# Kernel optimization log

Measured on AMD Instinct MI355X. Metric: run time of the kernel, lower is better.

Reference implementation:

```python
import jax, jax.numpy as jnp
import numpy as np

N = 8192
F_IN = 512
H = 512
E = 128
ALPHA = 0.2
NEG = -9e15


def _xavier(key, shape, gain=1.414):
    fan_in, fan_out = shape[0], shape[1]
    bound = gain * np.sqrt(6.0 / (fan_in + fan_out))
    return jax.random.uniform(key, shape, jnp.float32, -bound, bound)


def setup_inputs() -> dict:
    key = jax.random.key(0)
    ks = jax.random.split(key, 9)
    x = jax.random.normal(ks[0], (N, F_IN), jnp.float32)
    u = jax.random.uniform(ks[1], (N, N), jnp.float32)
    adj = jnp.where(u < 0.05, u, 0.0)
    M = jax.random.uniform(ks[2], (N, N), jnp.float32)
    return {
        "x": x, "adj": adj, "M": M,
        "W1": _xavier(ks[3], (F_IN, H)),
        "a_self1": _xavier(ks[4], (H, 1)),
        "a_neigh1": _xavier(ks[5], (H, 1)),
        "W2": _xavier(ks[6], (H, E)),
        "a_self2": _xavier(ks[7], (E, 1)),
        "a_neigh2": _xavier(ks[8], (E, 1)),
    }


def _gat_layer(x, adj, M, W, a_self, a_neigh):
    h = x @ W                                   # (N, out)
    s = h @ a_self                              # (N, 1)
    n = h @ a_neigh                             # (N, 1)
    e = (s + n.T) * M                           # (N, N) broadcast score sum
    e = jnp.where(e > 0, e, ALPHA * e)          # leaky_relu
    masked = jnp.where(adj > 0, e, NEG)
    attn = jax.nn.softmax(masked, axis=1)
    h_prime = attn @ h
    return jax.nn.elu(h_prime)


def reference(x, adj, M, W1, a_self1, a_neigh1, W2, a_self2, a_neigh2):
    h = _gat_layer(x, adj, M, W1, a_self1, a_neigh1)
    h = _gat_layer(h, adj, M, W2, a_self2, a_neigh2)
    z = h / jnp.maximum(jnp.linalg.norm(h, axis=1, keepdims=True), 1e-12)
    A_pred = jax.nn.sigmoid(z @ z.T)
    return (A_pred, z)
```

## Files before the change

kernel.cpp:

```cpp
#include <hip/hip_runtime.h>
#include <math.h>

#define NNODES 8192
#define CAP 1024

typedef __attribute__((ext_vector_type(8))) short bf16x8;
typedef __attribute__((ext_vector_type(4))) float f32x4;
typedef unsigned short ushort_t;

__device__ inline unsigned short f2bf(float x) {
    unsigned u = __builtin_bit_cast(unsigned, x);
    u += 0x7fffu + ((u >> 16) & 1u);
    return (unsigned short)(u >> 16);
}

#define GLOAD_LDS16(g, l)                                                      \
    __builtin_amdgcn_global_load_lds(                                          \
        (const __attribute__((address_space(1))) void*)(g),                    \
        (__attribute__((address_space(3))) void*)(l), 16, 0, 0)

template <int ROWS>
__device__ inline void stage_tile(ushort_t* lds, const ushort_t* g, size_t ld, int tid)
{
#pragma unroll
    for (int c = 0; c < ROWS / 32; ++c) {
        int row = c * 32 + (tid >> 3);
        int lch = (tid & 7) ^ (row & 7);
        GLOAD_LDS16(g + (size_t)row * ld + lch * 8, lds + (size_t)c * 2048 + tid * 8);
    }
}

__device__ inline int swz_off(int row, int kc) {
    return row * 64 + ((kc ^ (row & 7)) * 8);
}

__global__ __launch_bounds__(256) void gemm64(const float* __restrict__ A,
                                              const float* __restrict__ B,
                                              float* __restrict__ C,
                                              int M, int N, int K)
{
    __shared__ float sA[16][68];
    __shared__ float sB[16][68];

    const int tid = threadIdx.x;
    const int tx = tid & 15, ty = tid >> 4;
    const int bm = blockIdx.x * 64, bn = blockIdx.y * 64;

    float acc[4][4] = {};

    for (int k0 = 0; k0 < K; k0 += 16) {
        for (int l = tid; l < 64 * 16; l += 256) {
            int m = l >> 4, k = l & 15;
            sA[k][m] = A[(size_t)(bm + m) * K + k0 + k];
        }
        for (int l = tid; l < 16 * 64; l += 256) {
            int k = l >> 6, n = l & 63;
            sB[k][n] = B[(size_t)(k0 + k) * N + bn + n];
        }
        __syncthreads();
#pragma unroll
        for (int k = 0; k < 16; ++k) {
            float a[4], b[4];
#pragma unroll
            for (int i = 0; i < 4; ++i) a[i] = sA[k][ty * 4 + i];
#pragma unroll
            for (int j = 0; j < 4; ++j) b[j] = sB[k][tx * 4 + j];
#pragma unroll
            for (int i = 0; i < 4; ++i)
#pragma unroll
                for (int j = 0; j < 4; ++j) acc[i][j] += a[i] * b[j];
        }
        __syncthreads();
    }

#pragma unroll
    for (int i = 0; i < 4; ++i) {
        float4 v = make_float4(acc[i][0], acc[i][1], acc[i][2], acc[i][3]);
        *(float4*)&C[(size_t)(bm + ty * 4 + i) * N + bn + tx * 4] = v;
    }
}

template <int D>
__global__ __launch_bounds__(256) void sn_kernel(const float* __restrict__ h,
                                                 const float* __restrict__ a_s,
                                                 const float* __restrict__ a_n,
                                                 float* __restrict__ sv,
                                                 float* __restrict__ nv)
{
    const int row = (blockIdx.x * 256 + threadIdx.x) >> 6;
    const int lane = threadIdx.x & 63;
    if (row >= NNODES) return;
    const float* hr = h + (size_t)row * D;
    float a0 = 0.f, a1 = 0.f;
#pragma unroll
    for (int k = lane; k < D; k += 64) {
        float hv = hr[k];
        a0 += hv * a_s[k];
        a1 += hv * a_n[k];
    }
#pragma unroll
    for (int o = 32; o; o >>= 1) {
        a0 += __shfl_down(a0, o);
        a1 += __shfl_down(a1, o);
    }
    if (lane == 0) { sv[row] = a0; nv[row] = a1; }
}

__global__ __launch_bounds__(256) void build_csr(const float* __restrict__ adj,
                                                 const float* __restrict__ Mm,
                                                 unsigned short* __restrict__ cols,
                                                 float* __restrict__ vals,
                                                 int* __restrict__ nnzs)
{
    const int lane = threadIdx.x & 63;
    const int row = blockIdx.x * 4 + (threadIdx.x >> 6);
    const float4* arow = (const float4*)(adj + (size_t)row * NNODES);
    const float4* mrow = (const float4*)(Mm + (size_t)row * NNODES);
    const size_t base = (size_t)row * CAP;
    const unsigned long long below = (1ull << lane) - 1ull;

    int off = 0;
    for (int c4 = 0; c4 < NNODES / 4; c4 += 256) {
        float4 a[4], mv[4];
#pragma unroll
        for (int u = 0; u < 4; ++u) {
            a[u]  = arow[c4 + u * 64 + lane];
            mv[u] = mrow[c4 + u * 64 + lane];
        }
#pragma unroll
        for (int u = 0; u < 4; ++u) {
#pragma unroll
            for (int e = 0; e < 4; ++e) {
                float ae = (&a[u].x)[e];
                unsigned long long mask = __ballot(ae > 0.f);
                if (ae > 0.f) {
                    int pos = off + __popcll(mask & below);
                    if (pos < CAP) {
                        cols[base + pos] = (unsigned short)((c4 + u * 64 + lane) * 4 + e);
                        vals[base + pos] = (&mv[u].x)[e];
                    }
                }
                off += __popcll(mask);
            }
        }
    }
    if (lane == 0) nnzs[row] = off;
}

__global__ __launch_bounds__(256) void softmax_dense(const unsigned short* __restrict__ cols,
                                                     const float* __restrict__ vals,
                                                     const int* __restrict__ nnzs,
                                                     const float* __restrict__ sv,
                                                     const float* __restrict__ nv,
                                                     ushort_t* __restrict__ P)
{
    constexpr int NT = 256;
    __shared__ ushort_t drow[NNODES];
    __shared__ unsigned short scol[CAP];
    __shared__ float sp[CAP];
    __shared__ float reds[4];
    __shared__ float fb;

    const int tid = threadIdx.x;
    const int i = blockIdx.x;
    const int nnz = min(nnzs[i], CAP);
    const float si = sv[i];
    const size_t base = (size_t)i * CAP;

#pragma unroll
    for (int k = 0; k < NNODES / 8 / NT; ++k)
        ((uint4*)drow)[k * NT + tid] = (uint4){0u, 0u, 0u, 0u};

    float lmax = -3.0e38f;
    for (int k = tid; k < nnz; k += NT) {
        unsigned short c = cols[base + k];
        float e = (si + nv[c]) * vals[base + k];
        e = e > 0.f ? e : 0.2f * e;
        scol[k] = c;
        sp[k] = e;
        lmax = fmaxf(lmax, e);
    }
#pragma unroll
    for (int o = 32; o; o >>= 1) lmax = fmaxf(lmax, __shfl_down(lmax, o));
    if ((tid & 63) == 0) reds[tid >> 6] = lmax;
    __syncthreads();
    if (tid == 0) fb = fmaxf(fmaxf(reds[0], reds[1]), fmaxf(reds[2], reds[3]));
    __syncthreads();
    const float m = fb;

    float lsum = 0.f;
    for (int k = tid; k < nnz; k += NT) {
        float p = expf(sp[k] - m);
        sp[k] = p;
        lsum += p;
    }
#pragma unroll
    for (int o = 32; o; o >>= 1) lsum += __shfl_down(lsum, o);
    if ((tid & 63) == 0) reds[tid >> 6] = lsum;
    __syncthreads();
    if (tid == 0) fb = reds[0] + reds[1] + reds[2] + reds[3];
    __syncthreads();
    const float inv = 1.0f / fb;

    for (int k = tid; k < nnz; k += NT)
        drow[scol[k]] = f2bf(sp[k] * inv);
    __syncthreads();

    uint4* dst = (uint4*)(P + (size_t)i * NNODES);
#pragma unroll
    for (int k = 0; k < NNODES / 8 / NT; ++k)
        dst[k * NT + tid] = ((const uint4*)drow)[k * NT + tid];
}

__global__ __launch_bounds__(256) void tcast(const float* __restrict__ in,
                                             ushort_t* __restrict__ out,
                                             int R, int C)
{
    __shared__ ushort_t t[64][66];
    const int bi = blockIdx.x;
    const int bj = blockIdx.y;
    const int c = threadIdx.x & 63, r4 = threadIdx.x >> 6;
#pragma unroll
    for (int i = 0; i < 16; ++i) {
        int r = i * 4 + r4;
        t[r][c] = f2bf(in[(size_t)(bi * 64 + r) * C + bj * 64 + c]);
    }
    __syncthreads();
#pragma unroll
    for (int i = 0; i < 16; ++i) {
        int r = i * 4 + r4;
        out[(size_t)(bj * 64 + r) * R + bi * 64 + c] = t[c][r];
    }
}

__global__ __launch_bounds__(256) void cast_bf(const float* __restrict__ in,
                                               ushort_t* __restrict__ out, int n4)
{
    int i = blockIdx.x * 256 + threadIdx.x;
    if (i >= n4) return;
    float4 v = ((const float4*)in)[i];
    ushort_t o[4] = { f2bf(v.x), f2bf(v.y), f2bf(v.z), f2bf(v.w) };
    *(uint2*)&out[(size_t)i * 4] = *(uint2*)o;
}

template <int ELU>
__global__ __launch_bounds__(256) void gemm_mfma(const ushort_t* __restrict__ A,
                                                 const ushort_t* __restrict__ BT,
                                                 float* __restrict__ C,
                                                 int N, int K)
{
    __shared__ __align__(16) ushort_t At[128 * 64];
    __shared__ __align__(16) ushort_t Bt[128 * 64];

    const int tid = threadIdx.x;
    const int wid = tid >> 6, lane = tid & 63;
    const int wr = wid >> 1, wc = wid & 1;
    const int bm = blockIdx.x * 128;
    const int bn = blockIdx.y * 128;

    f32x4 acc[4][4] = {};

    for (int k0 = 0; k0 < K; k0 += 64) {
        stage_tile<128>(At, A + (size_t)bm * K + k0, K, tid);
        stage_tile<128>(Bt, BT + (size_t)bn * K + k0, K, tid);
        __syncthreads();
#pragma unroll
        for (int kk = 0; kk < 2; ++kk) {
            const int kc = kk * 4 + (lane >> 4);
            bf16x8 af[4], bfr[4];
#pragma unroll
            for (int m = 0; m < 4; ++m) {
                int r = wr * 64 + m * 16 + (lane & 15);
                af[m] = *(const bf16x8*)&At[swz_off(r, kc)];
            }
#pragma unroll
            for (int n = 0; n < 4; ++n) {
                int r = wc * 64 + n * 16 + (lane & 15);
                bfr[n] = *(const bf16x8*)&Bt[swz_off(r, kc)];
            }
#pragma unroll
            for (int m = 0; m < 4; ++m)
#pragma unroll
                for (int n = 0; n < 4; ++n)
                    acc[m][n] = __builtin_amdgcn_mfma_f32_16x16x32_bf16(af[m], bfr[n], acc[m][n], 0, 0, 0);
        }
        __syncthreads();
    }

#pragma unroll
    for (int m = 0; m < 4; ++m)
#pragma unroll
        for (int n = 0; n < 4; ++n)
#pragma unroll
            for (int r_ = 0; r_ < 4; ++r_) {
                int row = bm + wr * 64 + m * 16 + (lane >> 4) * 4 + r_;
                int col = bn + wc * 64 + n * 16 + (lane & 15);
                float v = acc[m][n][r_];
                if (ELU) v = v > 0.f ? v : expm1f(v);
                C[(size_t)row * N + col] = v;
            }
}

__global__ __launch_bounds__(256) void apred_mfma(const ushort_t* __restrict__ zb,
                                                  float* __restrict__ out)
{
    __shared__ __align__(16) ushort_t At[128 * 64];
    __shared__ __align__(16) ushort_t Bt[128 * 64];

    const int tid = threadIdx.x;
    const int wid = tid >> 6, lane = tid & 63;
    const int wr = wid >> 1, wc = wid & 1;
    const int bm = blockIdx.x * 128;
    const int bn = blockIdx.y * 128;

    f32x4 acc[4][4] = {};

#pragma unroll
    for (int k0 = 0; k0 < 128; k0 += 64) {
        stage_tile<128>(At, zb + (size_t)bm * 128 + k0, 128, tid);
        stage_tile<128>(Bt, zb + (size_t)bn * 128 + k0, 128, tid);
        __syncthreads();
#pragma unroll
        for (int kk = 0; kk < 2; ++kk) {
            const int kc = kk * 4 + (lane >> 4);
            bf16x8 af[4], bfr[4];
#pragma unroll
            for (int m = 0; m < 4; ++m) {
                int r = wr * 64 + m * 16 + (lane & 15);
                af[m] = *(const bf16x8*)&At[swz_off(r, kc)];
            }
#pragma unroll
            for (int n = 0; n < 4; ++n) {
                int r = wc * 64 + n * 16 + (lane & 15);
                bfr[n] = *(const bf16x8*)&Bt[swz_off(r, kc)];
            }
#pragma unroll
            for (int m = 0; m < 4; ++m)
#pragma unroll
                for (int n = 0; n < 4; ++n)
                    acc[m][n] = __builtin_amdgcn_mfma_f32_16x16x32_bf16(af[m], bfr[n], acc[m][n], 0, 0, 0);
        }
        __syncthreads();
    }

#pragma unroll
    for (int m = 0; m < 4; ++m)
#pragma unroll
        for (int n = 0; n < 4; ++n)
#pragma unroll
            for (int r_ = 0; r_ < 4; ++r_) {
                int row = bm + wr * 64 + m * 16 + (lane >> 4) * 4 + r_;
                int col = bn + wc * 64 + n * 16 + (lane & 15);
                float v = acc[m][n][r_];
                out[(size_t)row * NNODES + col] = 1.0f / (1.0f + expf(-v));
            }
}

__global__ __launch_bounds__(256) void attn2_csr(const unsigned short* __restrict__ cols,
                                                 const float* __restrict__ vals,
                                                 const int* __restrict__ nnzs,
                                                 const float* __restrict__ sv,
                                                 const float* __restrict__ nv,
                                                 const ushort_t* __restrict__ h2b,
                                                 float* __restrict__ out)
{
    constexpr int NT = 256;
    __shared__ unsigned short scol[CAP];
    __shared__ float sp[CAP];
    __shared__ float reds[4];
    __shared__ float fb;
    __shared__ float2 part[NT];

    const int tid = threadIdx.x;
    const int i = blockIdx.x;
    const int nnz = min(nnzs[i], CAP);
    const float si = sv[i];
    const size_t base = (size_t)i * CAP;

    float lmax = -3.0e38f;
    for (int k = tid; k < nnz; k += NT) {
        unsigned short c = cols[base + k];
        float e = (si + nv[c]) * vals[base + k];
        e = e > 0.f ? e : 0.2f * e;
        scol[k] = c;
        sp[k] = e;
        lmax = fmaxf(lmax, e);
    }
#pragma unroll
    for (int o = 32; o; o >>= 1) lmax = fmaxf(lmax, __shfl_down(lmax, o));
    if ((tid & 63) == 0) reds[tid >> 6] = lmax;
    __syncthreads();
    if (tid == 0) fb = fmaxf(fmaxf(reds[0], reds[1]), fmaxf(reds[2], reds[3]));
    __syncthreads();
    const float m = fb;

    float lsum = 0.f;
    for (int k = tid; k < nnz; k += NT) {
        float p = expf(sp[k] - m);
        sp[k] = p;
        lsum += p;
    }
#pragma unroll
    for (int o = 32; o; o >>= 1) lsum += __shfl_down(lsum, o);
    if ((tid & 63) == 0) reds[tid >> 6] = lsum;
    __syncthreads();
    if (tid == 0) fb = reds[0] + reds[1] + reds[2] + reds[3];
    __syncthreads();
    const float inv = 1.0f / fb;

    const int g = tid >> 6, lane = tid & 63;
    float ax = 0.f, ay = 0.f;
    for (int k = g; k < nnz; k += 4) {
        float pj = sp[k];
        unsigned hv = *(const unsigned*)&h2b[(size_t)scol[k] * 128 + lane * 2];
        ax += pj * __builtin_bit_cast(float, hv << 16);
        ay += pj * __builtin_bit_cast(float, hv & 0xffff0000u);
    }
    part[tid] = make_float2(ax, ay);
    __syncthreads();
    if (tid < 64) {
        float2 r0 = part[tid], r1 = part[tid + 64], r2 = part[tid + 128], r3 = part[tid + 192];
        float vx = (r0.x + r1.x + r2.x + r3.x) * inv;
        float vy = (r0.y + r1.y + r2.y + r3.y) * inv;
        out[(size_t)i * 128 + tid * 2]     = vx > 0.f ? vx : expm1f(vx);
        out[(size_t)i * 128 + tid * 2 + 1] = vy > 0.f ? vy : expm1f(vy);
    }
}

__global__ __launch_bounds__(256) void norm_kernel(const float* __restrict__ h,
                                                   float* __restrict__ z,
                                                   ushort_t* __restrict__ zb)
{
    const int row = (blockIdx.x * 256 + threadIdx.x) >> 6;
    const int lane = threadIdx.x & 63;
    if (row >= NNODES) return;
    const float* hr = h + (size_t)row * 128;
    float v0 = hr[lane], v1 = hr[lane + 64];
    float ss = v0 * v0 + v1 * v1;
#pragma unroll
    for (int o = 32; o; o >>= 1) ss += __shfl_down(ss, o);
    ss = __shfl(ss, 0);
    float invn = 1.0f / fmaxf(sqrtf(ss), 1e-12f);
    float z0 = v0 * invn, z1 = v1 * invn;
    z[(size_t)row * 128 + lane]      = z0;
    z[(size_t)row * 128 + lane + 64] = z1;
    zb[(size_t)row * 128 + lane]      = f2bf(z0);
    zb[(size_t)row * 128 + lane + 64] = f2bf(z1);
}

template <int D>
__global__ __launch_bounds__(256) void attn_kernel(const float* __restrict__ adj,
                                                   const float* __restrict__ Mm,
                                                   const float* __restrict__ sv,
                                                   const float* __restrict__ nv,
                                                   const float* __restrict__ h,
                                                   float* __restrict__ out)
{
    constexpr int NT = 256;
    constexpr int DCAP = 2048;
    __shared__ float pbuf[NNODES];
    __shared__ int   idxb[DCAP];
    __shared__ int   cnts[NT];
    __shared__ float reds[4];
    __shared__ float fbcast;
    __shared__ int   totc;

    const int tid = threadIdx.x;
    const int i = blockIdx.x;
    const size_t rowoff = (size_t)i * NNODES;
    const float si = sv[i];

    float lmax = -3.0e38f;
    for (int j = tid; j < NNODES; j += NT) {
        float a = adj[rowoff + j];
        float val = -9.0e15f;
        if (a > 0.f) {
            float e = (si + nv[j]) * Mm[rowoff + j];
            val = e > 0.f ? e : 0.2f * e;
            lmax = fmaxf(lmax, val);
        }
        pbuf[j] = val;
    }
#pragma unroll
    for (int o = 32; o; o >>= 1) lmax = fmaxf(lmax, __shfl_down(lmax, o));
    if ((tid & 63) == 0) reds[tid >> 6] = lmax;
    __syncthreads();
    if (tid == 0) fbcast = fmaxf(fmaxf(reds[0], reds[1]), fmaxf(reds[2], reds[3]));
    __syncthreads();
    const float m = fbcast;

    float lsum = 0.f;
    int myc = 0;
    for (int j = tid; j < NNODES; j += NT) {
        float v = pbuf[j];
        float p = (v > -8.9e15f) ? expf(v - m) : 0.f;
        pbuf[j] = p;
        lsum += p;
        if (p > 0.f) myc++;
    }
#pragma unroll
    for (int o = 32; o; o >>= 1) lsum += __shfl_down(lsum, o);
    if ((tid & 63) == 0) reds[tid >> 6] = lsum;
    cnts[tid] = myc;
    __syncthreads();
    if (tid == 0) {
        fbcast = reds[0] + reds[1] + reds[2] + reds[3];
        int run = 0;
        for (int t = 0; t < NT; ++t) { int c = cnts[t]; cnts[t] = run; run += c; }
        totc = run;
    }
    __syncthreads();
    const float inv = 1.0f / fbcast;
    const int nnz = totc;

    if (nnz <= DCAP) {
        int off = cnts[tid];
        for (int j = tid; j < NNODES; j += NT)
            if (pbuf[j] > 0.f) idxb[off++] = j;
    }
    __syncthreads();

    if constexpr (D == 512) {
        const int c = tid;
        float acc0 = 0.f, acc1 = 0.f;
        if (nnz <= DCAP) {
#pragma unroll 4
            for (int t = 0; t < nnz; ++t) {
                int j = idxb[t];
                float pj = pbuf[j];
                const float* hr = h + (size_t)j * 512;
                acc0 += pj * hr[c];
                acc1 += pj * hr[c + 256];
            }
        } else {
            for (int j = 0; j < NNODES; ++j) {
                float pj = pbuf[j];
                if (pj > 0.f) {
                    const float* hr = h + (size_t)j * 512;
                    acc0 += pj * hr[c];
                    acc1 += pj * hr[c + 256];
                }
            }
        }
        float r0 = acc0 * inv, r1 = acc1 * inv;
        out[(size_t)i * 512 + c]       = r0 > 0.f ? r0 : expm1f(r0);
        out[(size_t)i * 512 + c + 256] = r1 > 0.f ? r1 : expm1f(r1);
    } else {
        const int half = tid >> 7;
        const int c = tid & 127;
        float acc = 0.f;
        if (nnz <= DCAP) {
#pragma unroll 4
            for (int t = half; t < nnz; t += 2) {
                int j = idxb[t];
                acc += pbuf[j] * h[(size_t)j * 128 + c];
            }
        } else {
            for (int j = half; j < NNODES; j += 2) {
                float pj = pbuf[j];
                if (pj > 0.f) acc += pj * h[(size_t)j * 128 + c];
            }
        }
        __syncthreads();
        pbuf[tid] = acc;
        __syncthreads();
        if (tid < 128) {
            float r = (pbuf[tid] + pbuf[tid + 128]) * inv;
            out[(size_t)i * 128 + tid] = r > 0.f ? r : expm1f(r);
        }
    }
}

__global__ __launch_bounds__(256) void apred_kernel(const float* __restrict__ z,
                                                    float* __restrict__ out)
{
    __shared__ float sA[32][68];
    __shared__ float sB[32][68];

    const int tid = threadIdx.x;
    const int tx = tid & 15, ty = tid >> 4;
    const int bm = blockIdx.x * 64, bn = blockIdx.y * 64;

    float acc[4][4] = {};

    for (int k0 = 0; k0 < 128; k0 += 32) {
        for (int l = tid; l < 64 * 32; l += 256) {
            int r = l >> 5, kk = l & 31;
            sA[kk][r] = z[(size_t)(bm + r) * 128 + k0 + kk];
            sB[kk][r] = z[(size_t)(bn + r) * 128 + k0 + kk];
        }
        __syncthreads();
#pragma unroll
        for (int kk = 0; kk < 32; ++kk) {
            float a[4], b[4];
#pragma unroll
            for (int i = 0; i < 4; ++i) a[i] = sA[kk][ty * 4 + i];
#pragma unroll
            for (int j = 0; j < 4; ++j) b[j] = sB[kk][tx * 4 + j];
#pragma unroll
            for (int i = 0; i < 4; ++i)
#pragma unroll
                for (int j = 0; j < 4; ++j) acc[i][j] += a[i] * b[j];
        }
        __syncthreads();
    }

#pragma unroll
    for (int i = 0; i < 4; ++i) {
        float4 v;
        v.x = 1.0f / (1.0f + expf(-acc[i][0]));
        v.y = 1.0f / (1.0f + expf(-acc[i][1]));
        v.z = 1.0f / (1.0f + expf(-acc[i][2]));
        v.w = 1.0f / (1.0f + expf(-acc[i][3]));
        *(float4*)&out[(size_t)(bm + ty * 4 + i) * NNODES + bn + tx * 4] = v;
    }
}

extern "C" void kernel_launch(void* const* d_in, const int* in_sizes, int n_in,
                              void* d_out, int out_size, void* d_ws, size_t ws_size,
                              hipStream_t stream)
{
    const float* x   = (const float*)d_in[0];
    const float* adj = (const float*)d_in[1];
    const float* Mm  = (const float*)d_in[2];
    const float* W1  = (const float*)d_in[3];
    const float* as1 = (const float*)d_in[4];
    const float* an1 = (const float*)d_in[5];
    const float* W2  = (const float*)d_in[6];
    const float* as2 = (const float*)d_in[7];
    const float* an2 = (const float*)d_in[8];

    float* out   = (float*)d_out;
    float* Apred = out;
    float* z     = out + (size_t)NNODES * NNODES;

    ushort_t* P   = (ushort_t*)Apred;
    ushort_t* hbT = (ushort_t*)((char*)Apred + (size_t)134217728);

    float* ws  = (float*)d_ws;
    float* h1  = ws;
    float* h1p = h1 + (size_t)NNODES * 512;
    float* h2p = h1p + (size_t)NNODES * 512;
    float* sv  = h2p + (size_t)NNODES * 128;
    float* nv  = sv + NNODES;
    float* vals = nv + NNODES;
    unsigned short* cols = (unsigned short*)(vals + (size_t)NNODES * CAP);
    int* nnzs = (int*)(cols + (size_t)NNODES * CAP);
    ushort_t* zb  = (ushort_t*)(nnzs + NNODES);
    ushort_t* h2b = zb + (size_t)NNODES * 128;
    ushort_t* xb  = h2b + (size_t)NNODES * 128;
    ushort_t* W1T = xb + (size_t)NNODES * 512;

    const size_t need = (size_t)((char*)(W1T + 512 * 512) - (char*)d_ws);

    if (ws_size >= need) {
        build_csr<<<dim3(2048), 256, 0, stream>>>(adj, Mm, cols, vals, nnzs);

        cast_bf<<<dim3(4096), 256, 0, stream>>>(x, xb, NNODES * 512 / 4);
        tcast<<<dim3(8, 8), 256, 0, stream>>>(W1, W1T, 512, 512);
        gemm_mfma<0><<<dim3(64, 4), 256, 0, stream>>>(xb, W1T, h1, 512, 512);
        sn_kernel<512><<<dim3(2048), 256, 0, stream>>>(h1, as1, an1, sv, nv);
        softmax_dense<<<dim3(NNODES), 256, 0, stream>>>(cols, vals, nnzs, sv, nv, P);
        tcast<<<dim3(128, 8), 256, 0, stream>>>(h1, hbT, NNODES, 512);
        gemm_mfma<1><<<dim3(64, 4), 256, 0, stream>>>(P, hbT, h1p, 512, NNODES);

        gemm64<<<dim3(128, 2), 256, 0, stream>>>(h1p, W2, h1, NNODES, 128, 512);
        sn_kernel<128><<<dim3(2048), 256, 0, stream>>>(h1, as2, an2, sv, nv);
        cast_bf<<<dim3(1024), 256, 0, stream>>>(h1, h2b, NNODES * 128 / 4);
        attn2_csr<<<dim3(NNODES), 256, 0, stream>>>(cols, vals, nnzs, sv, nv, h2b, h2p);

        norm_kernel<<<dim3(2048), 256, 0, stream>>>(h2p, z, zb);
        apred_mfma<<<dim3(64, 64), 256, 0, stream>>>(zb, Apred);
    } else {
        gemm64<<<dim3(128, 8), 256, 0, stream>>>((const float*)d_in[0], W1, h1, NNODES, 512, 512);
        sn_kernel<512><<<dim3(2048), 256, 0, stream>>>(h1, as1, an1, sv, nv);
        attn_kernel<512><<<dim3(NNODES), 256, 0, stream>>>(adj, Mm, sv, nv, h1, h1p);

        gemm64<<<dim3(128, 2), 256, 0, stream>>>(h1p, W2, h1, NNODES, 128, 512);
        sn_kernel<128><<<dim3(2048), 256, 0, stream>>>(h1, as2, an2, sv, nv);
        attn_kernel<128><<<dim3(NNODES), 256, 0, stream>>>(adj, Mm, sv, nv, h1, h2p);

        norm_kernel<<<dim3(2048), 256, 0, stream>>>(h2p, z, zb);
        apred_kernel<<<dim3(128, 128), 256, 0, stream>>>(z, Apred);
    }
}
```

Baseline: 627.0 us.

## Fuse CSR construction into dense attention-score softmax kernel

Replaces the separate build_csr and softmax_dense kernels with one per-row kernel. It reads adj and M densely, computes the masked leaky-relu scores into LDS, runs the softmax, and writes the bf16 probability row straight to P. It then rebuilds the CSR (cols, vals, nnzs) for layer 2 with a block-wide prefix scan, re-reading M values for the retained edges. This removes one kernel launch and the round trip through the CSR buffers for layer 1, but adds a scan with many barriers, a scattered second read of M, and CSR columns that are no longer in sorted order.

```diff
diff --git a/kernel.cpp b/kernel.cpp
--- a/kernel.cpp
+++ b/kernel.cpp
@@ -106,79 +106,49 @@
     if (lane == 0) { sv[row] = a0; nv[row] = a1; }
 }
 
-__global__ __launch_bounds__(256) void build_csr(const float* __restrict__ adj,
-                                                 const float* __restrict__ Mm,
-                                                 unsigned short* __restrict__ cols,
-                                                 float* __restrict__ vals,
-                                                 int* __restrict__ nnzs)
-{
-    const int lane = threadIdx.x & 63;
-    const int row = blockIdx.x * 4 + (threadIdx.x >> 6);
-    const float4* arow = (const float4*)(adj + (size_t)row * NNODES);
-    const float4* mrow = (const float4*)(Mm + (size_t)row * NNODES);
-    const size_t base = (size_t)row * CAP;
-    const unsigned long long below = (1ull << lane) - 1ull;
-
-    int off = 0;
-    for (int c4 = 0; c4 < NNODES / 4; c4 += 256) {
-        float4 a[4], mv[4];
-#pragma unroll
-        for (int u = 0; u < 4; ++u) {
-            a[u]  = arow[c4 + u * 64 + lane];
-            mv[u] = mrow[c4 + u * 64 + lane];
-        }
-#pragma unroll
-        for (int u = 0; u < 4; ++u) {
-#pragma unroll
-            for (int e = 0; e < 4; ++e) {
-                float ae = (&a[u].x)[e];
-                unsigned long long mask = __ballot(ae > 0.f);
-                if (ae > 0.f) {
-                    int pos = off + __popcll(mask & below);
-                    if (pos < CAP) {
-                        cols[base + pos] = (unsigned short)((c4 + u * 64 + lane) * 4 + e);
-                        vals[base + pos] = (&mv[u].x)[e];
-                    }
-                }
-                off += __popcll(mask);
-            }
-        }
-    }
-    if (lane == 0) nnzs[row] = off;
-}
-
-__global__ __launch_bounds__(256) void softmax_dense(const unsigned short* __restrict__ cols,
-                                                     const float* __restrict__ vals,
-                                                     const int* __restrict__ nnzs,
-                                                     const float* __restrict__ sv,
-                                                     const float* __restrict__ nv,
-                                                     ushort_t* __restrict__ P)
+__global__ __launch_bounds__(256) void escore_fused(const float* __restrict__ adj,
+                                                    const float* __restrict__ Mm,
+                                                    const float* __restrict__ sv,
+                                                    const float* __restrict__ nv,
+                                                    unsigned short* __restrict__ cols,
+                                                    float* __restrict__ vals,
+                                                    int* __restrict__ nnzs,
+                                                    ushort_t* __restrict__ P)
 {
     constexpr int NT = 256;
-    __shared__ ushort_t drow[NNODES];
-    __shared__ unsigned short scol[CAP];
-    __shared__ float sp[CAP];
+    constexpr int NF = NNODES / 4 / NT;
+    __shared__ float ebuf[NNODES];
+    __shared__ int   scan[NT];
     __shared__ float reds[4];
     __shared__ float fb;
 
     const int tid = threadIdx.x;
     const int i = blockIdx.x;
-    const int nnz = min(nnzs[i], CAP);
+    const size_t rowoff = (size_t)i * NNODES;
     const float si = sv[i];
-    const size_t base = (size_t)i * CAP;
-
-#pragma unroll
-    for (int k = 0; k < NNODES / 8 / NT; ++k)
-        ((uint4*)drow)[k * NT + tid] = (uint4){0u, 0u, 0u, 0u};
+    const float4* a4p = (const float4*)(adj + rowoff);
+    const float4* m4p = (const float4*)(Mm + rowoff);
+    float4* e4p = (float4*)ebuf;
 
     float lmax = -3.0e38f;
-    for (int k = tid; k < nnz; k += NT) {
-        unsigned short c = cols[base + k];
-        float e = (si + nv[c]) * vals[base + k];
-        e = e > 0.f ? e : 0.2f * e;
-        scol[k] = c;
-        sp[k] = e;
-        lmax = fmaxf(lmax, e);
+#pragma unroll
+    for (int k = 0; k < NF; ++k) {
+        int f = k * NT + tid;
+        float4 a = a4p[f];
+        float4 mv = m4p[f];
+        float4 ev;
+#pragma unroll
+        for (int e = 0; e < 4; ++e) {
+            float ae = (&a.x)[e];
+            float val = -9.0e15f;
+            if (ae > 0.f) {
+                float t = (si + nv[f * 4 + e]) * (&mv.x)[e];
+                val = t > 0.f ? t : 0.2f * t;
+                lmax = fmaxf(lmax, val);
+            }
+            (&ev.x)[e] = val;
+        }
+        e4p[f] = ev;
     }
 #pragma unroll
     for (int o = 32; o; o >>= 1) lmax = fmaxf(lmax, __shfl_down(lmax, o));
@@ -189,10 +159,19 @@
     const float m = fb;
 
     float lsum = 0.f;
-    for (int k = tid; k < nnz; k += NT) {
-        float p = expf(sp[k] - m);
-        sp[k] = p;
-        lsum += p;
+#pragma unroll
+    for (int k = 0; k < NF; ++k) {
+        int f = k * NT + tid;
+        float4 ev = e4p[f];
+        float4 pv;
+#pragma unroll
+        for (int e = 0; e < 4; ++e) {
+            float v = (&ev.x)[e];
+            float p = (v > -8.9e15f) ? expf(v - m) : 0.f;
+            (&pv.x)[e] = p;
+            lsum += p;
+        }
+        e4p[f] = pv;
     }
 #pragma unroll
     for (int o = 32; o; o >>= 1) lsum += __shfl_down(lsum, o);
@@ -200,16 +179,52 @@
     __syncthreads();
     if (tid == 0) fb = reds[0] + reds[1] + reds[2] + reds[3];
     __syncthreads();
-    const float inv = 1.0f / fb;
-
-    for (int k = tid; k < nnz; k += NT)
-        drow[scol[k]] = f2bf(sp[k] * inv);
-    __syncthreads();
-
-    uint4* dst = (uint4*)(P + (size_t)i * NNODES);
-#pragma unroll
-    for (int k = 0; k < NNODES / 8 / NT; ++k)
-        dst[k * NT + tid] = ((const uint4*)drow)[k * NT + tid];
+    const float inv = fb > 0.f ? 1.0f / fb : 0.f;
+
+#pragma unroll
+    for (int k = 0; k < NF; ++k) {
+        int f = k * NT + tid;
+        float4 pv = e4p[f];
+        ushort_t o4[4] = { f2bf(pv.x * inv), f2bf(pv.y * inv),
+                           f2bf(pv.z * inv), f2bf(pv.w * inv) };
+        *(uint2*)&P[rowoff + (size_t)f * 4] = *(uint2*)o4;
+    }
+
+    int cnt = 0;
+#pragma unroll
+    for (int k = 0; k < NF; ++k) {
+        float4 pv = e4p[k * NT + tid];
+#pragma unroll
+        for (int e = 0; e < 4; ++e) cnt += ((&pv.x)[e] > 0.f) ? 1 : 0;
+    }
+    scan[tid] = cnt;
+    __syncthreads();
+    for (int o = 1; o < NT; o <<= 1) {
+        int v = (tid >= o) ? scan[tid - o] : 0;
+        __syncthreads();
+        scan[tid] += v;
+        __syncthreads();
+    }
+    int off = scan[tid] - cnt;
+    if (tid == NT - 1) nnzs[i] = scan[tid];
+
+    const size_t base = (size_t)i * CAP;
+#pragma unroll
+    for (int k = 0; k < NF; ++k) {
+        int f = k * NT + tid;
+        float4 pv = e4p[f];
+#pragma unroll
+        for (int e = 0; e < 4; ++e) {
+            if ((&pv.x)[e] > 0.f) {
+                if (off < CAP) {
+                    int col = f * 4 + e;
+                    cols[base + off] = (unsigned short)col;
+                    vals[base + off] = Mm[rowoff + col];
+                }
+                ++off;
+            }
+        }
+    }
 }
 
 __global__ __launch_bounds__(256) void tcast(const float* __restrict__ in,
@@ -654,13 +669,14 @@
     const size_t need = (size_t)((char*)(W1T + 512 * 512) - (char*)d_ws);
 
     if (ws_size >= need) {
-        build_csr<<<dim3(2048), 256, 0, stream>>>(adj, Mm, cols, vals, nnzs);
-
         cast_bf<<<dim3(4096), 256, 0, stream>>>(x, xb, NNODES * 512 / 4);
         tcast<<<dim3(8, 8), 256, 0, stream>>>(W1, W1T, 512, 512);
         gemm_mfma<0><<<dim3(64, 4), 256, 0, stream>>>(xb, W1T, h1, 512, 512);
         sn_kernel<512><<<dim3(2048), 256, 0, stream>>>(h1, as1, an1, sv, nv);
-        softmax_dense<<<dim3(NNODES), 256, 0, stream>>>(cols, vals, nnzs, sv, nv, P);
+
+        escore_fused<<<dim3(NNODES), 256, 0, stream>>>(adj, Mm, sv, nv,
+                                                       cols, vals, nnzs, P);
+
         tcast<<<dim3(128, 8), 256, 0, stream>>>(h1, hbT, NNODES, 512);
         gemm_mfma<1><<<dim3(64, 4), 256, 0, stream>>>(P, hbT, h1p, 512, NNODES);
 
@@ -672,7 +688,7 @@
         norm_kernel<<<dim3(2048), 256, 0, stream>>>(h2p, z, zb);
         apred_mfma<<<dim3(64, 64), 256, 0, stream>>>(zb, Apred);
     } else {
-        gemm64<<<dim3(128, 8), 256, 0, stream>>>((const float*)d_in[0], W1, h1, NNODES, 512, 512);
+        gemm64<<<dim3(128, 8), 256, 0, stream>>>(x, W1, h1, NNODES, 512, 512);
         sn_kernel<512><<<dim3(2048), 256, 0, stream>>>(h1, as1, an1, sv, nv);
         attn_kernel<512><<<dim3(NNODES), 256, 0, stream>>>(adj, Mm, sv, nv, h1, h1p);
 
```

Result: slower. 780.7 us (+24.5%).
